# Performance work log

Hardware: AMD Instinct MI355X
Metric: run time of the kernel (lower is better)

Reference implementation:

```python
import jax, jax.numpy as jnp
import numpy as np

B, N, D, NS, ITERS = 32, 2048, 512, 8, 3
EPS = 1e-8
SCALE = D ** -0.5
LN_EPS = 1e-5


def _ln(x, g, b):
    m = x.mean(-1, keepdims=True)
    v = ((x - m) ** 2).mean(-1, keepdims=True)
    return (x - m) * jax.lax.rsqrt(v + LN_EPS) * g + b


def setup_inputs() -> dict:
    key = jax.random.key(0)
    ks = iter(jax.random.split(key, 40))
    w = lambda *s: jax.random.normal(next(ks), s, jnp.float32) * 0.02
    inp = {
        'inputs': jax.random.normal(next(ks), (B, N, D), jnp.float32),
        'slot_noise': jax.random.normal(next(ks), (B, NS, D), jnp.float32),
        'slots_mu': jax.random.normal(next(ks), (1, 1, D), jnp.float32),
        'slots_logsigma': w(1, 1, D),
        'k_w': w(D, D), 'k_b': jnp.zeros((D,), jnp.float32),
        'v_w': w(D, D), 'v_b': jnp.zeros((D,), jnp.float32),
        'gru_w_ih': w(3 * D, D), 'gru_w_hh': w(3 * D, D),
        'gru_b_ih': jnp.zeros((3 * D,), jnp.float32),
        'gru_b_hh': jnp.zeros((3 * D,), jnp.float32),
        'ln_in_g': jnp.ones((D,), jnp.float32), 'ln_in_b': jnp.zeros((D,), jnp.float32),
        'ln_slots_g': jnp.ones((D,), jnp.float32), 'ln_slots_b': jnp.zeros((D,), jnp.float32),
        'ln_pre_g': jnp.ones((D,), jnp.float32), 'ln_pre_b': jnp.zeros((D,), jnp.float32),
        'mlp1_w': w(1024, D), 'mlp1_b': jnp.zeros((1024,), jnp.float32),
        'mlp2_w': w(1024, 1024), 'mlp2_b': jnp.zeros((1024,), jnp.float32),
        'mlp3_w': w(512, 1024), 'mlp3_b': jnp.zeros((512,), jnp.float32),
        'mlp4_w': w(256, 512), 'mlp4_b': jnp.zeros((256,), jnp.float32),
    }
    return inp


def reference(inputs, slot_noise, slots_mu, slots_logsigma, k_w, k_b, v_w, v_b,
              gru_w_ih, gru_w_hh, gru_b_ih, gru_b_hh,
              ln_in_g, ln_in_b, ln_slots_g, ln_slots_b, ln_pre_g, ln_pre_b,
              mlp1_w, mlp1_b, mlp2_w, mlp2_b, mlp3_w, mlp3_b, mlp4_w, mlp4_b):
    b, n, d = inputs.shape
    # stochastic slot init: mu + exp(logsigma) * noise  -> [b, ns, d]
    slots = slots_mu + jnp.exp(slots_logsigma) * slot_noise
    x = _ln(inputs, ln_in_g, ln_in_b)
    k = x @ k_w.T + k_b
    v = x @ v_w.T + v_b
    updates = slots
    for _ in range(ITERS):
        slots_prev = slots
        q = _ln(slots, ln_slots_g, ln_slots_b)
        dots = jnp.einsum('bid,bjd->bij', q, k) * SCALE  # [b, ns, n]
        attn = jax.nn.softmax(dots, axis=1) + EPS        # softmax over slot axis
        attn = attn / attn.sum(-1, keepdims=True)        # renorm over tokens
        updates = jnp.einsum('bjd,bij->bid', v, attn)    # [b, ns, d]
        # GRUCell(updates, slots_prev), then residual add of updates
        u = updates.reshape(-1, d)
        h = slots_prev.reshape(-1, d)
        gi = u @ gru_w_ih.T + gru_b_ih
        gh = h @ gru_w_hh.T + gru_b_hh
        i_r, i_z, i_n = jnp.split(gi, 3, axis=-1)
        h_r, h_z, h_n = jnp.split(gh, 3, axis=-1)
        r = jax.nn.sigmoid(i_r + h_r)
        z = jax.nn.sigmoid(i_z + h_z)
        nn_ = jnp.tanh(i_n + r * h_n)
        h_new = (1.0 - z) * nn_ + z * h
        slots = (u + h_new).reshape(b, -1, d)
    # output MLP with exact GELU (torch default)
    s = _ln(slots, ln_pre_g, ln_pre_b)
    s = jax.nn.gelu(s @ mlp1_w.T + mlp1_b, approximate=False)
    s = jax.nn.gelu(s @ mlp2_w.T + mlp2_b, approximate=False)
    s = jax.nn.gelu(s @ mlp3_w.T + mlp3_b, approximate=False)
    s = s @ mlp4_w.T + mlp4_b
    return (updates, s)
```

## Files before the change

### kernel.cpp

```cpp
#include <hip/hip_runtime.h>
#include <math.h>

#define Bb 32
#define Nn 2048
#define Dd 512
#define NS 8
#define ITERS 3
#define EPSf 1e-8f
#define SCALEf 0.04419417382415922f
#define LN_EPSf 1e-5f

#define QHS 520
#define PTS 72
#define CHUNKS 32

typedef _Float16 half8 __attribute__((ext_vector_type(8)));
typedef _Float16 half4 __attribute__((ext_vector_type(4)));
typedef float f32x4 __attribute__((ext_vector_type(4)));

__device__ __forceinline__ float waveReduceSum(float v) {
    #pragma unroll
    for (int m = 32; m >= 1; m >>= 1) v += __shfl_xor(v, m);
    return v;
}

__device__ __forceinline__ float gelu_exact(float x) {
    return 0.5f * x * (1.0f + erff(x * 0.7071067811865476f));
}

__device__ __forceinline__ void async_copy16(const _Float16* g, _Float16* l) {
    __builtin_amdgcn_global_load_lds(
        (const __attribute__((address_space(1))) unsigned int*)g,
        (__attribute__((address_space(3))) unsigned int*)l, 16, 0, 0);
}

__global__ __launch_bounds__(256) void megapack_kernel(
    const float* __restrict__ k_w, const float* __restrict__ v_w,
    const float* __restrict__ w_ih, const float* __restrict__ w_hh,
    const float* __restrict__ m1, const float* __restrict__ m2,
    const float* __restrict__ m3, const float* __restrict__ m4,
    _Float16* __restrict__ Bkv, _Float16* __restrict__ Bih, _Float16* __restrict__ Bhh,
    _Float16* __restrict__ Bm1, _Float16* __restrict__ Bm2,
    _Float16* __restrict__ Bm3, _Float16* __restrict__ Bm4) {
    int bid = blockIdx.x, tid = threadIdx.x;
    const float* src; _Float16* dst; int kbits, base;
    if (bid < 2048) {
        int i = bid * 256 + tid;
        Bkv[i] = (_Float16)(i < 262144 ? k_w[i] : v_w[i - 262144]);
        return;
    }
    else if (bid < 5120)  { src = w_ih; dst = Bih; kbits = 9;  base = 2048; }
    else if (bid < 8192)  { src = w_hh; dst = Bhh; kbits = 9;  base = 5120; }
    else if (bid < 10240) { src = m1;   dst = Bm1; kbits = 9;  base = 8192; }
    else if (bid < 14336) { src = m2;   dst = Bm2; kbits = 10; base = 10240; }
    else if (bid < 16384) { src = m3;   dst = Bm3; kbits = 10; base = 14336; }
    else                  { src = m4;   dst = Bm4; kbits = 9;  base = 16384; }
    int e = (bid - base) * 256 + tid;
    int K = 1 << kbits;
    int row = e >> kbits, k = e & (K - 1);
    _Float16 h = (_Float16)src[e];
    _Float16* d = dst + ((size_t)row << (kbits + 1));
    d[k] = h;
    d[K + k] = h;
}

__global__ __launch_bounds__(256) void pack_ln_single_kernel(
    const float* __restrict__ x, const float* __restrict__ g, const float* __restrict__ b,
    _Float16* __restrict__ Ap) {
    int wid = blockIdx.x * 4 + (threadIdx.x >> 6);
    int lane = threadIdx.x & 63;
    const float4* row4 = (const float4*)(x + (size_t)wid * Dd);
    float4 va = row4[lane * 2], vb = row4[lane * 2 + 1];
    float v[8] = {va.x, va.y, va.z, va.w, vb.x, vb.y, vb.z, vb.w};
    float s = 0.f, sq = 0.f;
    #pragma unroll
    for (int t = 0; t < 8; ++t) { s += v[t]; sq += v[t] * v[t]; }
    s = waveReduceSum(s);
    sq = waveReduceSum(sq);
    float m = s * (1.0f / Dd);
    float var = sq * (1.0f / Dd) - m * m;
    float rs = rsqrtf(var + LN_EPSf);
    const float4* g4 = (const float4*)g;
    const float4* b4 = (const float4*)b;
    float4 ga = g4[lane * 2], gb = g4[lane * 2 + 1];
    float4 ba = b4[lane * 2], bb = b4[lane * 2 + 1];
    float gg[8] = {ga.x, ga.y, ga.z, ga.w, gb.x, gb.y, gb.z, gb.w};
    float bbv[8] = {ba.x, ba.y, ba.z, ba.w, bb.x, bb.y, bb.z, bb.w};
    half8 o;
    #pragma unroll
    for (int t = 0; t < 8; ++t) o[t] = (_Float16)((v[t] - m) * rs * gg[t] + bbv[t]);
    *(half8*)(Ap + (size_t)wid * Dd + lane * 8) = o;
}

__global__ __launch_bounds__(256) void slots_init_kernel(
    const float* __restrict__ noise, const float* __restrict__ mu,
    const float* __restrict__ ls, float* __restrict__ slots, _Float16* __restrict__ A2) {
    int idx = blockIdx.x * 256 + threadIdx.x;
    if (idx >= Bb * NS * Dd) return;
    int d = idx & (Dd - 1);
    float val = mu[d] + expf(ls[d]) * noise[idx];
    slots[idx] = val;
    int row = idx >> 9;
    _Float16 hi = (_Float16)val;
    A2[(size_t)(256 + row) * 1024 + d] = hi;
    A2[(size_t)(256 + row) * 1024 + 512 + d] = (_Float16)(val - (float)hi);
}

__device__ __forceinline__ void hgemm128_core(
    const _Float16* __restrict__ A, const _Float16* __restrict__ Bw,
    int K2, f32x4 acc[4][4], _Float16* As, _Float16* Bs) {
    const int tid = threadIdx.x;
    const int w = tid >> 6, lane = tid & 63;
    const int r8 = lane >> 3, seg = lane & 7;
    const int lr = lane & 15, quad = lane >> 4;
    const int wm = w >> 1, wn = w & 1;
    for (int k0 = 0; k0 < K2; k0 += 64) {
        __syncthreads();
        #pragma unroll
        for (int g = 0; g < 4; ++g) {
            int grp = w * 4 + g;
            int row = grp * 8 + r8;
            async_copy16(A + (size_t)row * K2 + k0 + seg * 8, As + grp * 512);
            async_copy16(Bw + (size_t)row * K2 + k0 + seg * 8, Bs + grp * 512);
        }
        __syncthreads();
        #pragma unroll
        for (int kk = 0; kk < 2; ++kk) {
            half8 a[4], b[4];
            #pragma unroll
            for (int t = 0; t < 4; ++t) {
                a[t] = *(const half8*)(As + (wm * 64 + t * 16 + lr) * 64 + kk * 32 + quad * 8);
                b[t] = *(const half8*)(Bs + (wn * 64 + t * 16 + lr) * 64 + kk * 32 + quad * 8);
            }
            #pragma unroll
            for (int mt = 0; mt < 4; ++mt)
                #pragma unroll
                for (int nt = 0; nt < 4; ++nt)
                    acc[mt][nt] = __builtin_amdgcn_mfma_f32_16x16x32_f16(
                        a[mt], b[nt], acc[mt][nt], 0, 0, 0);
        }
    }
}

__global__ __launch_bounds__(256) void kv_hgemm_kernel(
    const _Float16* __restrict__ Apack, const _Float16* __restrict__ Bkv,
    const float* __restrict__ k_b, const float* __restrict__ v_b,
    _Float16* __restrict__ khalf, _Float16* __restrict__ vT) {
    __shared__ _Float16 smem[17408];
    _Float16* As = smem;
    _Float16* Bs = smem + 8192;
    const int f = blockIdx.x;
    const int m0 = ((f & 7) + ((f >> 6) << 3)) * 128;
    const int n0 = ((f >> 3) & 7) * 128;
    f32x4 acc[4][4];
    #pragma unroll
    for (int i = 0; i < 4; ++i)
        #pragma unroll
        for (int j = 0; j < 4; ++j) acc[i][j] = (f32x4){0.f, 0.f, 0.f, 0.f};
    hgemm128_core(Apack + (size_t)m0 * 512, Bkv + (size_t)n0 * 512, 512, acc, As, Bs);
    __syncthreads();
    const int tid = threadIdx.x;
    const int w = tid >> 6, lane = tid & 63;
    const int lr = lane & 15, quad = lane >> 4;
    const int wm = w >> 1, wn = w & 1;
    const bool isK = (n0 < 512);
    #pragma unroll
    for (int mt = 0; mt < 4; ++mt)
        #pragma unroll
        for (int nt = 0; nt < 4; ++nt) {
            int ml = wm * 64 + mt * 16 + quad * 4;
            int nl = wn * 64 + nt * 16 + lr;
            float bv = isK ? k_b[n0 + nl] : v_b[n0 - 512 + nl];
            #pragma unroll
            for (int r = 0; r < 4; ++r) {
                _Float16 h = (_Float16)(acc[mt][nt][r] + bv);
                if (isK) smem[(ml + r) * 136 + nl] = h;
                else     smem[nl * 136 + ml + r] = h;
            }
        }
    __syncthreads();
    int r = tid >> 1, half = tid & 1;
    _Float16* dst;
    if (isK) {
        dst = khalf + (size_t)(m0 + r) * 512 + n0 + half * 64;
    } else {
        int b = m0 >> 11, j0 = m0 & 2047, d0 = n0 - 512;
        dst = vT + ((size_t)b * 512 + d0 + r) * 2048 + j0 + half * 64;
    }
    #pragma unroll
    for (int c = 0; c < 8; ++c)
        *(half8*)(dst + c * 8) = *(const half8*)(smem + r * 136 + half * 64 + c * 8);
}

__global__ __launch_bounds__(256) void attn_kernel(
    const float* __restrict__ slots, const float* __restrict__ ln_g, const float* __restrict__ ln_b,
    const _Float16* __restrict__ khalf, const _Float16* __restrict__ vT,
    float* __restrict__ rawp, float* __restrict__ sumsp) {
    const int b = blockIdx.y, chunk = blockIdx.x;
    __shared__ _Float16 qh[16 * QHS];
    __shared__ _Float16 pT[16 * PTS];
    __shared__ float sums_lds[64];
    const int tid = threadIdx.x, w = tid >> 6, lane = tid & 63;
    const int lr = lane & 15, quad = lane >> 4;

    #pragma unroll
    for (int rr = 0; rr < 2; ++rr) {
        int row = w * 2 + rr;
        const float* sr = slots + ((size_t)b * NS + row) * Dd;
        float v[8]; float s = 0.f, sq = 0.f;
        #pragma unroll
        for (int t = 0; t < 8; ++t) {
            v[t] = sr[t * 64 + lane];
            s += v[t]; sq += v[t] * v[t];
        }
        s = waveReduceSum(s);
        sq = waveReduceSum(sq);
        float m = s * (1.0f / Dd);
        float var = sq * (1.0f / Dd) - m * m;
        float rs = rsqrtf(var + LN_EPSf);
        #pragma unroll
        for (int t = 0; t < 8; ++t) {
            int d = t * 64 + lane;
            qh[row * QHS + d] = (_Float16)(((v[t] - m) * rs * ln_g[d] + ln_b[d]) * SCALEf);
            qh[(row + 8) * QHS + d] = (_Float16)0.f;
        }
    }
    __syncthreads();

    const int j0 = chunk * 64 + w * 16;
    f32x4 dots = (f32x4){0.f, 0.f, 0.f, 0.f};
    for (int ks = 0; ks < 16; ++ks) {
        half8 bq = *(const half8*)(qh + lr * QHS + ks * 32 + quad * 8);
        half8 ak = *(const half8*)(khalf + ((size_t)b * Nn + j0 + lr) * 512 + ks * 32 + quad * 8);
        dots = __builtin_amdgcn_mfma_f32_16x16x32_f16(ak, bq, dots, 0, 0, 0);
    }
    float ssum = 0.f;
    {
        f32x4 d = dots;
        f32x4 mx = d;
        #pragma unroll
        for (int msk = 1; msk <= 4; msk <<= 1) {
            #pragma unroll
            for (int r = 0; r < 4; ++r) mx[r] = fmaxf(mx[r], __shfl_xor(mx[r], msk));
        }
        f32x4 p;
        #pragma unroll
        for (int r = 0; r < 4; ++r) p[r] = __expf(d[r] - mx[r]);
        f32x4 sm = p;
        #pragma unroll
        for (int msk = 1; msk <= 4; msk <<= 1) {
            #pragma unroll
            for (int r = 0; r < 4; ++r) sm[r] += __shfl_xor(sm[r], msk);
        }
        #pragma unroll
        for (int r = 0; r < 4; ++r) {
            _Float16 ph = (_Float16)(p[r] / sm[r] + EPSf);
            pT[lr * PTS + w * 16 + quad * 4 + r] = ph;
            ssum += (float)ph;
        }
    }
    ssum += __shfl_xor(ssum, 16);
    ssum += __shfl_xor(ssum, 32);
    if (lane < 16) sums_lds[w * 16 + lane] = ssum;
    __syncthreads();

    f32x4 acc[8];
    #pragma unroll
    for (int nf = 0; nf < 8; ++nf) acc[nf] = (f32x4){0.f, 0.f, 0.f, 0.f};
    #pragma unroll
    for (int kc = 0; kc < 2; ++kc) {
        half8 ap = *(const half8*)(pT + lr * PTS + kc * 32 + quad * 8);
        #pragma unroll
        for (int nf = 0; nf < 8; ++nf) {
            int dcol = w * 128 + nf * 16 + lr;
            half8 bv = *(const half8*)(vT + ((size_t)b * 512 + dcol) * 2048 + chunk * 64 + kc * 32 + quad * 8);
            acc[nf] = __builtin_amdgcn_mfma_f32_16x16x32_f16(ap, bv, acc[nf], 0, 0, 0);
        }
    }
    if (quad < 2) {
        #pragma unroll
        for (int nf = 0; nf < 8; ++nf) {
            #pragma unroll
            for (int r = 0; r < 4; ++r) {
                int slot = quad * 4 + r;
                rawp[(((size_t)chunk * Bb + b) * NS + slot) * Dd + w * 128 + nf * 16 + lr] = acc[nf][r];
            }
        }
    }
    if (w == 0 && lane < NS) {
        float tot = sums_lds[lane] + sums_lds[16 + lane] + sums_lds[32 + lane] + sums_lds[48 + lane];
        sumsp[((size_t)chunk * Bb + b) * NS + lane] = tot;
    }
}

__global__ __launch_bounds__(256) void finalize_kernel(
    const float* __restrict__ rawp, const float* __restrict__ sumsp,
    float* __restrict__ u, float* __restrict__ out0, _Float16* __restrict__ A2) {
    int idx = blockIdx.x * 256 + threadIdx.x;
    int row = idx >> 9, k = idx & 511;
    float rs = 0.f, ss = 0.f;
    #pragma unroll
    for (int c = 0; c < CHUNKS; ++c) {
        rs += rawp[(size_t)c * 131072 + idx];
        ss += sumsp[c * 256 + row];
    }
    float val = rs / ss;
    u[idx] = val;
    out0[idx] = val;
    _Float16 hi = (_Float16)val;
    A2[(size_t)row * 1024 + k] = hi;
    A2[(size_t)row * 1024 + 512 + k] = (_Float16)(val - (float)hi);
}

__device__ __forceinline__ void hgemm64_core(
    const _Float16* __restrict__ A, const _Float16* __restrict__ Bw,
    int K2, f32x4 acc[2][2], _Float16* As, _Float16* Bs) {
    const int tid = threadIdx.x;
    const int w = tid >> 6, lane = tid & 63;
    const int r8 = lane >> 3, seg = lane & 7;
    const int lr = lane & 15, quad = lane >> 4;
    const int wm = w >> 1, wn = w & 1;
    for (int k0 = 0; k0 < K2; k0 += 64) {
        __syncthreads();
        #pragma unroll
        for (int p = 0; p < 2; ++p) {
            int grp = p * 4 + w;
            int row = grp * 8 + r8;
            async_copy16(A + (size_t)row * K2 + k0 + seg * 8, As + grp * 512);
            async_copy16(Bw + (size_t)row * K2 + k0 + seg * 8, Bs + grp * 512);
        }
        __syncthreads();
        #pragma unroll
        for (int kk = 0; kk < 2; ++kk) {
            half8 a[2], b[2];
            #pragma unroll
            for (int t = 0; t < 2; ++t) {
                a[t] = *(const half8*)(As + (wm * 32 + t * 16 + lr) * 64 + kk * 32 + quad * 8);
                b[t] = *(const half8*)(Bs + (wn * 32 + t * 16 + lr) * 64 + kk * 32 + quad * 8);
            }
            #pragma unroll
            for (int mt = 0; mt < 2; ++mt)
                #pragma unroll
                for (int nt = 0; nt < 2; ++nt)
                    acc[mt][nt] = __builtin_amdgcn_mfma_f32_16x16x32_f16(
                        a[mt], b[nt], acc[mt][nt], 0, 0, 0);
        }
    }
}

template <int ACT, int PACK>
__global__ __launch_bounds__(256) void hgemm64_kernel(
    const _Float16* __restrict__ A, const _Float16* __restrict__ Bw,
    const float* __restrict__ bias, float* __restrict__ C, _Float16* __restrict__ P,
    int K2, int N, int Kp) {
    __shared__ _Float16 As[4096], Bs[4096];
    const int m0 = blockIdx.y * 64, n0 = blockIdx.x * 64;
    f32x4 acc[2][2];
    #pragma unroll
    for (int i = 0; i < 2; ++i)
        #pragma unroll
        for (int j = 0; j < 2; ++j) acc[i][j] = (f32x4){0.f, 0.f, 0.f, 0.f};
    hgemm64_core(A + (size_t)m0 * K2, Bw + (size_t)n0 * K2, K2, acc, As, Bs);
    const int tid = threadIdx.x;
    const int w = tid >> 6, lane = tid & 63;
    const int lr = lane & 15, quad = lane >> 4;
    const int wm = w >> 1, wn = w & 1;
    #pragma unroll
    for (int mt = 0; mt < 2; ++mt)
        #pragma unroll
        for (int nt = 0; nt < 2; ++nt) {
            int n = n0 + wn * 32 + nt * 16 + lr;
            float bv = bias[n];
            #pragma unroll
            for (int r = 0; r < 4; ++r) {
                int m = m0 + wm * 32 + mt * 16 + quad * 4 + r;
                float val = acc[mt][nt][r] + bv;
                if (ACT) val = gelu_exact(val);
                if (PACK) {
                    _Float16 hi = (_Float16)val;
                    P[(size_t)m * 2 * Kp + n] = hi;
                    P[(size_t)m * 2 * Kp + Kp + n] = (_Float16)(val - (float)hi);
                } else {
                    C[(size_t)m * N + n] = val;
                }
            }
        }
}

__global__ __launch_bounds__(256) void gru_gemm_kernel(
    const _Float16* __restrict__ A2, const _Float16* __restrict__ Bih,
    const _Float16* __restrict__ Bhh, const float* __restrict__ b_ih,
    const float* __restrict__ b_hh, float* __restrict__ gi, float* __restrict__ gh) {
    __shared__ _Float16 As[4096], Bs[4096];
    const int by = blockIdx.y;
    const int n0 = blockIdx.x * 64;
    const _Float16* Ap; const _Float16* Bw; const float* bias; float* C;
    if (by < 4) { Ap = A2 + (size_t)by * 64 * 1024;        Bw = Bih; bias = b_ih; C = gi + (size_t)by * 64 * 1536; }
    else        { Ap = A2 + (size_t)(256 + (by - 4) * 64) * 1024; Bw = Bhh; bias = b_hh; C = gh + (size_t)(by - 4) * 64 * 1536; }
    f32x4 acc[2][2];
    #pragma unroll
    for (int i = 0; i < 2; ++i)
        #pragma unroll
        for (int j = 0; j < 2; ++j) acc[i][j] = (f32x4){0.f, 0.f, 0.f, 0.f};
    hgemm64_core(Ap, Bw + (size_t)n0 * 1024, 1024, acc, As, Bs);
    const int tid = threadIdx.x;
    const int w = tid >> 6, lane = tid & 63;
    const int lr = lane & 15, quad = lane >> 4;
    const int wm = w >> 1, wn = w & 1;
    #pragma unroll
    for (int mt = 0; mt < 2; ++mt)
        #pragma unroll
        for (int nt = 0; nt < 2; ++nt) {
            int n = n0 + wn * 32 + nt * 16 + lr;
            float bv = bias[n];
            #pragma unroll
            for (int r = 0; r < 4; ++r) {
                int m = wm * 32 + mt * 16 + quad * 4 + r;
                C[(size_t)m * 1536 + n] = acc[mt][nt][r] + bv;
            }
        }
}

__global__ __launch_bounds__(256) void gru_elem_kernel(
    const float* __restrict__ gi, const float* __restrict__ gh,
    const float* __restrict__ u, float* __restrict__ slots, _Float16* __restrict__ A2,
    const float* __restrict__ lnp_g, const float* __restrict__ lnp_b,
    _Float16* __restrict__ P1, int last) {
    int row = blockIdx.x * 4 + (threadIdx.x >> 6);
    int lane = threadIdx.x & 63;
    const float* gir = gi + (size_t)row * 1536;
    const float* ghr = gh + (size_t)row * 1536;
    float val[8];
    #pragma unroll
    for (int t = 0; t < 8; ++t) {
        int d = t * 64 + lane;
        float ir = gir[d], iz = gir[512 + d], in_ = gir[1024 + d];
        float hr = ghr[d], hz = ghr[512 + d], hn = ghr[1024 + d];
        float r = 1.0f / (1.0f + expf(-(ir + hr)));
        float z = 1.0f / (1.0f + expf(-(iz + hz)));
        float n = tanhf(in_ + r * hn);
        float h = slots[(size_t)row * 512 + d];
        float hnew = (1.0f - z) * n + z * h;
        float vv = u[(size_t)row * 512 + d] + hnew;
        val[t] = vv;
        slots[(size_t)row * 512 + d] = vv;
        _Float16 hi = (_Float16)vv;
        A2[(size_t)(256 + row) * 1024 + d] = hi;
        A2[(size_t)(256 + row) * 1024 + 512 + d] = (_Float16)(vv - (float)hi);
    }
    if (last) {
        float s = 0.f, sq = 0.f;
        #pragma unroll
        for (int t = 0; t < 8; ++t) { s += val[t]; sq += val[t] * val[t]; }
        s = waveReduceSum(s);
        sq = waveReduceSum(sq);
        float m = s * (1.0f / Dd);
        float var = sq * (1.0f / Dd) - m * m;
        float rs = rsqrtf(var + LN_EPSf);
        #pragma unroll
        for (int t = 0; t < 8; ++t) {
            int d = t * 64 + lane;
            float a = (val[t] - m) * rs * lnp_g[d] + lnp_b[d];
            _Float16 hi = (_Float16)a;
            P1[(size_t)row * 1024 + d] = hi;
            P1[(size_t)row * 1024 + 512 + d] = (_Float16)(a - (float)hi);
        }
    }
}

extern "C" void kernel_launch(void* const* d_in, const int* in_sizes, int n_in,
                              void* d_out, int out_size, void* d_ws, size_t ws_size,
                              hipStream_t stream) {
    const float* inputs   = (const float*)d_in[0];
    const float* noise    = (const float*)d_in[1];
    const float* mu       = (const float*)d_in[2];
    const float* lsig     = (const float*)d_in[3];
    const float* k_w      = (const float*)d_in[4];
    const float* k_b      = (const float*)d_in[5];
    const float* v_w      = (const float*)d_in[6];
    const float* v_b      = (const float*)d_in[7];
    const float* w_ih     = (const float*)d_in[8];
    const float* w_hh     = (const float*)d_in[9];
    const float* b_ih     = (const float*)d_in[10];
    const float* b_hh     = (const float*)d_in[11];
    const float* ln_in_g  = (const float*)d_in[12];
    const float* ln_in_b  = (const float*)d_in[13];
    const float* ln_s_g   = (const float*)d_in[14];
    const float* ln_s_b   = (const float*)d_in[15];
    const float* ln_p_g   = (const float*)d_in[16];
    const float* ln_p_b   = (const float*)d_in[17];
    const float* mlp1_w   = (const float*)d_in[18];
    const float* mlp1_b   = (const float*)d_in[19];
    const float* mlp2_w   = (const float*)d_in[20];
    const float* mlp2_b   = (const float*)d_in[21];
    const float* mlp3_w   = (const float*)d_in[22];
    const float* mlp3_b   = (const float*)d_in[23];
    const float* mlp4_w   = (const float*)d_in[24];
    const float* mlp4_b   = (const float*)d_in[25];
    float* out0 = (float*)d_out;
    float* out1 = (float*)d_out + Bb * NS * Dd;

    char* wp = (char*)d_ws;
    auto alloc = [&](size_t bytes) -> void* {
        void* p = (void*)wp;
        wp += (bytes + 255) & ~(size_t)255;
        return p;
    };
    const size_t MR = (size_t)Bb * Nn;
    _Float16* Apack = (_Float16*)alloc(MR * 512 * 2);
    _Float16* khalf = (_Float16*)alloc(MR * 512 * 2);
    _Float16* vT    = (_Float16*)alloc((size_t)Bb * 512 * Nn * 2);
    _Float16* Bkv   = (_Float16*)alloc((size_t)1024 * 512 * 2);
    _Float16* Bih   = (_Float16*)alloc((size_t)1536 * 1024 * 2);
    _Float16* Bhh   = (_Float16*)alloc((size_t)1536 * 1024 * 2);
    _Float16* Bm1   = (_Float16*)alloc((size_t)1024 * 1024 * 2);
    _Float16* Bm2   = (_Float16*)alloc((size_t)1024 * 2048 * 2);
    _Float16* Bm3   = (_Float16*)alloc((size_t)512 * 2048 * 2);
    _Float16* Bm4   = (_Float16*)alloc((size_t)256 * 1024 * 2);
    float* slots    = (float*)alloc((size_t)Bb * NS * Dd * 4);
    float* rawp     = (float*)alloc((size_t)CHUNKS * Bb * NS * Dd * 4);
    float* sumsp    = (float*)alloc((size_t)CHUNKS * Bb * NS * 4);
    float* ubuf     = (float*)alloc((size_t)Bb * NS * Dd * 4);
    float* gi       = (float*)alloc((size_t)Bb * NS * 1536 * 4);
    float* gh       = (float*)alloc((size_t)Bb * NS * 1536 * 4);
    _Float16* A2    = (_Float16*)alloc((size_t)512 * 1024 * 2);
    _Float16* P1    = (_Float16*)alloc((size_t)256 * 1024 * 2);
    _Float16* P2    = (_Float16*)alloc((size_t)256 * 2048 * 2);
    _Float16* P3    = (_Float16*)alloc((size_t)256 * 2048 * 2);
    _Float16* P4    = (_Float16*)alloc((size_t)256 * 1024 * 2);

    megapack_kernel<<<16896, 256, 0, stream>>>(
        k_w, v_w, w_ih, w_hh, mlp1_w, mlp2_w, mlp3_w, mlp4_w,
        Bkv, Bih, Bhh, Bm1, Bm2, Bm3, Bm4);
    pack_ln_single_kernel<<<MR / 4, 256, 0, stream>>>(inputs, ln_in_g, ln_in_b, Apack);
    slots_init_kernel<<<(Bb * NS * Dd) / 256, 256, 0, stream>>>(noise, mu, lsig, slots, A2);

    kv_hgemm_kernel<<<4096, 256, 0, stream>>>(Apack, Bkv, k_b, v_b, khalf, vT);

    for (int it = 0; it < ITERS; ++it) {
        attn_kernel<<<dim3(CHUNKS, Bb), 256, 0, stream>>>(slots, ln_s_g, ln_s_b, khalf, vT, rawp, sumsp);
        finalize_kernel<<<512, 256, 0, stream>>>(rawp, sumsp, ubuf, out0, A2);
        gru_gemm_kernel<<<dim3(24, 8), 256, 0, stream>>>(A2, Bih, Bhh, b_ih, b_hh, gi, gh);
        gru_elem_kernel<<<64, 256, 0, stream>>>(gi, gh, ubuf, slots, A2,
                                                ln_p_g, ln_p_b, P1, it == ITERS - 1 ? 1 : 0);
    }

    hgemm64_kernel<1, 1><<<dim3(16, 4), 256, 0, stream>>>(P1, Bm1, mlp1_b, nullptr, P2, 1024, 1024, 1024);
    hgemm64_kernel<1, 1><<<dim3(16, 4), 256, 0, stream>>>(P2, Bm2, mlp2_b, nullptr, P3, 2048, 1024, 1024);
    hgemm64_kernel<1, 1><<<dim3(8, 4), 256, 0, stream>>>(P3, Bm3, mlp3_b, nullptr, P4, 2048, 512, 512);
    hgemm64_kernel<0, 0><<<dim3(4, 4), 256, 0, stream>>>(P4, Bm4, mlp4_b, out1, nullptr, 1024, 256, 256);
}
```

Baseline: 681.4 us.

## Enlarge KV GEMM tile to 256x128 and drop LDS staging in small GEMMs

The K/V projection GEMM moves from 128x128 to 256x128 tiles with 8x4 MFMA accumulators per wave, halving the grid. The epilogue is now written out in two 128-row passes through shared memory. The small GRU and MLP GEMMs drop LDS staging and __syncthreads, so each wave loads its MFMA fragments straight from global memory. This cuts barrier and launch overhead on latency-bound small GEMMs but raises register pressure in the KV kernel and loses cross-wave reuse of the global loads.

```diff
diff --git a/kernel.cpp b/kernel.cpp
--- a/kernel.cpp
+++ b/kernel.cpp
@@ -15,7 +15,6 @@
 #define CHUNKS 32
 
 typedef _Float16 half8 __attribute__((ext_vector_type(8)));
-typedef _Float16 half4 __attribute__((ext_vector_type(4)));
 typedef float f32x4 __attribute__((ext_vector_type(4)));
 
 __device__ __forceinline__ float waveReduceSum(float v) {
@@ -106,90 +105,93 @@
     A2[(size_t)(256 + row) * 1024 + 512 + d] = (_Float16)(val - (float)hi);
 }
 
-__device__ __forceinline__ void hgemm128_core(
-    const _Float16* __restrict__ A, const _Float16* __restrict__ Bw,
-    int K2, f32x4 acc[4][4], _Float16* As, _Float16* Bs) {
+__global__ __launch_bounds__(256) void kv_hgemm_kernel(
+    const _Float16* __restrict__ Apack, const _Float16* __restrict__ Bkv,
+    const float* __restrict__ k_b, const float* __restrict__ v_b,
+    _Float16* __restrict__ khalf, _Float16* __restrict__ vT) {
+    __shared__ _Float16 smem[24576];
+    _Float16* As = smem;
+    _Float16* Bs = smem + 16384;
+    const int f = blockIdx.x;
+    const int m0 = ((f & 7) + ((f >> 6) << 3)) * 256;
+    const int n0 = ((f >> 3) & 7) * 128;
     const int tid = threadIdx.x;
     const int w = tid >> 6, lane = tid & 63;
     const int r8 = lane >> 3, seg = lane & 7;
     const int lr = lane & 15, quad = lane >> 4;
     const int wm = w >> 1, wn = w & 1;
-    for (int k0 = 0; k0 < K2; k0 += 64) {
+
+    f32x4 acc[8][4];
+    #pragma unroll
+    for (int i = 0; i < 8; ++i)
+        #pragma unroll
+        for (int j = 0; j < 4; ++j) acc[i][j] = (f32x4){0.f, 0.f, 0.f, 0.f};
+
+    for (int k0 = 0; k0 < 512; k0 += 64) {
         __syncthreads();
         #pragma unroll
-        for (int g = 0; g < 4; ++g) {
-            int grp = w * 4 + g;
-            int row = grp * 8 + r8;
-            async_copy16(A + (size_t)row * K2 + k0 + seg * 8, As + grp * 512);
-            async_copy16(Bw + (size_t)row * K2 + k0 + seg * 8, Bs + grp * 512);
+        for (int g = 0; g < 12; ++g) {
+            int grp = w * 12 + g;
+            if (grp < 32) {
+                int row = grp * 8 + r8;
+                async_copy16(Apack + (size_t)(m0 + row) * 512 + k0 + seg * 8, As + grp * 512);
+            } else {
+                int brow = (grp - 32) * 8 + r8;
+                async_copy16(Bkv + (size_t)(n0 + brow) * 512 + k0 + seg * 8, Bs + (grp - 32) * 512);
+            }
         }
         __syncthreads();
         #pragma unroll
         for (int kk = 0; kk < 2; ++kk) {
-            half8 a[4], b[4];
-            #pragma unroll
-            for (int t = 0; t < 4; ++t) {
-                a[t] = *(const half8*)(As + (wm * 64 + t * 16 + lr) * 64 + kk * 32 + quad * 8);
-                b[t] = *(const half8*)(Bs + (wn * 64 + t * 16 + lr) * 64 + kk * 32 + quad * 8);
-            }
-            #pragma unroll
-            for (int mt = 0; mt < 4; ++mt)
+            half8 a[8], b[4];
+            #pragma unroll
+            for (int t = 0; t < 8; ++t)
+                a[t] = *(const half8*)(As + (wm * 128 + t * 16 + lr) * 64 + kk * 32 + quad * 8);
+            #pragma unroll
+            for (int u = 0; u < 4; ++u)
+                b[u] = *(const half8*)(Bs + (wn * 64 + u * 16 + lr) * 64 + kk * 32 + quad * 8);
+            #pragma unroll
+            for (int mt = 0; mt < 8; ++mt)
                 #pragma unroll
                 for (int nt = 0; nt < 4; ++nt)
                     acc[mt][nt] = __builtin_amdgcn_mfma_f32_16x16x32_f16(
                         a[mt], b[nt], acc[mt][nt], 0, 0, 0);
         }
     }
-}
-
-__global__ __launch_bounds__(256) void kv_hgemm_kernel(
-    const _Float16* __restrict__ Apack, const _Float16* __restrict__ Bkv,
-    const float* __restrict__ k_b, const float* __restrict__ v_b,
-    _Float16* __restrict__ khalf, _Float16* __restrict__ vT) {
-    __shared__ _Float16 smem[17408];
-    _Float16* As = smem;
-    _Float16* Bs = smem + 8192;
-    const int f = blockIdx.x;
-    const int m0 = ((f & 7) + ((f >> 6) << 3)) * 128;
-    const int n0 = ((f >> 3) & 7) * 128;
-    f32x4 acc[4][4];
-    #pragma unroll
-    for (int i = 0; i < 4; ++i)
-        #pragma unroll
-        for (int j = 0; j < 4; ++j) acc[i][j] = (f32x4){0.f, 0.f, 0.f, 0.f};
-    hgemm128_core(Apack + (size_t)m0 * 512, Bkv + (size_t)n0 * 512, 512, acc, As, Bs);
-    __syncthreads();
-    const int tid = threadIdx.x;
-    const int w = tid >> 6, lane = tid & 63;
-    const int lr = lane & 15, quad = lane >> 4;
-    const int wm = w >> 1, wn = w & 1;
     const bool isK = (n0 < 512);
-    #pragma unroll
-    for (int mt = 0; mt < 4; ++mt)
-        #pragma unroll
-        for (int nt = 0; nt < 4; ++nt) {
-            int ml = wm * 64 + mt * 16 + quad * 4;
-            int nl = wn * 64 + nt * 16 + lr;
-            float bv = isK ? k_b[n0 + nl] : v_b[n0 - 512 + nl];
-            #pragma unroll
-            for (int r = 0; r < 4; ++r) {
-                _Float16 h = (_Float16)(acc[mt][nt][r] + bv);
-                if (isK) smem[(ml + r) * 136 + nl] = h;
-                else     smem[nl * 136 + ml + r] = h;
-            }
-        }
-    __syncthreads();
-    int r = tid >> 1, half = tid & 1;
-    _Float16* dst;
-    if (isK) {
-        dst = khalf + (size_t)(m0 + r) * 512 + n0 + half * 64;
-    } else {
-        int b = m0 >> 11, j0 = m0 & 2047, d0 = n0 - 512;
-        dst = vT + ((size_t)b * 512 + d0 + r) * 2048 + j0 + half * 64;
-    }
-    #pragma unroll
-    for (int c = 0; c < 8; ++c)
-        *(half8*)(dst + c * 8) = *(const half8*)(smem + r * 136 + half * 64 + c * 8);
+    const int bidx = m0 >> 11;
+    #pragma unroll
+    for (int p = 0; p < 2; ++p) {
+        __syncthreads();
+        if (wm == p) {
+            #pragma unroll
+            for (int mt = 0; mt < 8; ++mt)
+                #pragma unroll
+                for (int nt = 0; nt < 4; ++nt) {
+                    int ml = mt * 16 + quad * 4;
+                    int nl = wn * 64 + nt * 16 + lr;
+                    float bv = isK ? k_b[n0 + nl] : v_b[n0 - 512 + nl];
+                    #pragma unroll
+                    for (int r = 0; r < 4; ++r) {
+                        _Float16 h = (_Float16)(acc[mt][nt][r] + bv);
+                        if (isK) smem[(ml + r) * 136 + nl] = h;
+                        else     smem[nl * 136 + ml + r] = h;
+                    }
+                }
+        }
+        __syncthreads();
+        int r = tid >> 1, half = tid & 1;
+        _Float16* dst;
+        if (isK) {
+            dst = khalf + (size_t)(m0 + p * 128 + r) * 512 + n0 + half * 64;
+        } else {
+            int j0 = (m0 & 2047) + p * 128;
+            dst = vT + ((size_t)bidx * 512 + (n0 - 512) + r) * 2048 + j0 + half * 64;
+        }
+        #pragma unroll
+        for (int c = 0; c < 8; ++c)
+            *(half8*)(dst + c * 8) = *(const half8*)(smem + r * 136 + half * 64 + c * 8);
+    }
 }
 
 __global__ __launch_bounds__(256) void attn_kernel(
@@ -312,68 +314,51 @@
     A2[(size_t)row * 1024 + 512 + k] = (_Float16)(val - (float)hi);
 }
 
-__device__ __forceinline__ void hgemm64_core(
+__device__ __forceinline__ void sgemm_tile(
     const _Float16* __restrict__ A, const _Float16* __restrict__ Bw,
-    int K2, f32x4 acc[2][2], _Float16* As, _Float16* Bs) {
-    const int tid = threadIdx.x;
-    const int w = tid >> 6, lane = tid & 63;
-    const int r8 = lane >> 3, seg = lane & 7;
+    int m0w, int n0w, int K2, f32x4 acc[2][2]) {
+    const int lane = threadIdx.x & 63;
     const int lr = lane & 15, quad = lane >> 4;
-    const int wm = w >> 1, wn = w & 1;
-    for (int k0 = 0; k0 < K2; k0 += 64) {
-        __syncthreads();
-        #pragma unroll
-        for (int p = 0; p < 2; ++p) {
-            int grp = p * 4 + w;
-            int row = grp * 8 + r8;
-            async_copy16(A + (size_t)row * K2 + k0 + seg * 8, As + grp * 512);
-            async_copy16(Bw + (size_t)row * K2 + k0 + seg * 8, Bs + grp * 512);
-        }
-        __syncthreads();
-        #pragma unroll
-        for (int kk = 0; kk < 2; ++kk) {
-            half8 a[2], b[2];
-            #pragma unroll
-            for (int t = 0; t < 2; ++t) {
-                a[t] = *(const half8*)(As + (wm * 32 + t * 16 + lr) * 64 + kk * 32 + quad * 8);
-                b[t] = *(const half8*)(Bs + (wn * 32 + t * 16 + lr) * 64 + kk * 32 + quad * 8);
-            }
-            #pragma unroll
-            for (int mt = 0; mt < 2; ++mt)
-                #pragma unroll
-                for (int nt = 0; nt < 2; ++nt)
-                    acc[mt][nt] = __builtin_amdgcn_mfma_f32_16x16x32_f16(
-                        a[mt], b[nt], acc[mt][nt], 0, 0, 0);
-        }
+    const _Float16* Ap = A + (size_t)(m0w + lr) * K2 + quad * 8;
+    const _Float16* Bp = Bw + (size_t)(n0w + lr) * K2 + quad * 8;
+    const int steps = K2 >> 5;
+    #pragma unroll 4
+    for (int ks = 0; ks < steps; ++ks) {
+        half8 a0 = *(const half8*)(Ap + ks * 32);
+        half8 a1 = *(const half8*)(Ap + (size_t)16 * K2 + ks * 32);
+        half8 b0 = *(const half8*)(Bp + ks * 32);
+        half8 b1 = *(const half8*)(Bp + (size_t)16 * K2 + ks * 32);
+        acc[0][0] = __builtin_amdgcn_mfma_f32_16x16x32_f16(a0, b0, acc[0][0], 0, 0, 0);
+        acc[0][1] = __builtin_amdgcn_mfma_f32_16x16x32_f16(a0, b1, acc[0][1], 0, 0, 0);
+        acc[1][0] = __builtin_amdgcn_mfma_f32_16x16x32_f16(a1, b0, acc[1][0], 0, 0, 0);
+        acc[1][1] = __builtin_amdgcn_mfma_f32_16x16x32_f16(a1, b1, acc[1][1], 0, 0, 0);
     }
 }
 
 template <int ACT, int PACK>
-__global__ __launch_bounds__(256) void hgemm64_kernel(
+__global__ __launch_bounds__(256) void sgemm_kernel(
     const _Float16* __restrict__ A, const _Float16* __restrict__ Bw,
     const float* __restrict__ bias, float* __restrict__ C, _Float16* __restrict__ P,
     int K2, int N, int Kp) {
-    __shared__ _Float16 As[4096], Bs[4096];
-    const int m0 = blockIdx.y * 64, n0 = blockIdx.x * 64;
-    f32x4 acc[2][2];
-    #pragma unroll
-    for (int i = 0; i < 2; ++i)
-        #pragma unroll
-        for (int j = 0; j < 2; ++j) acc[i][j] = (f32x4){0.f, 0.f, 0.f, 0.f};
-    hgemm64_core(A + (size_t)m0 * K2, Bw + (size_t)n0 * K2, K2, acc, As, Bs);
     const int tid = threadIdx.x;
     const int w = tid >> 6, lane = tid & 63;
     const int lr = lane & 15, quad = lane >> 4;
     const int wm = w >> 1, wn = w & 1;
+    f32x4 acc[2][2];
+    #pragma unroll
+    for (int i = 0; i < 2; ++i)
+        #pragma unroll
+        for (int j = 0; j < 2; ++j) acc[i][j] = (f32x4){0.f, 0.f, 0.f, 0.f};
+    sgemm_tile(A, Bw, blockIdx.y * 64 + wm * 32, blockIdx.x * 64 + wn * 32, K2, acc);
     #pragma unroll
     for (int mt = 0; mt < 2; ++mt)
         #pragma unroll
         for (int nt = 0; nt < 2; ++nt) {
-            int n = n0 + wn * 32 + nt * 16 + lr;
+            int n = blockIdx.x * 64 + wn * 32 + nt * 16 + lr;
             float bv = bias[n];
             #pragma unroll
             for (int r = 0; r < 4; ++r) {
-                int m = m0 + wm * 32 + mt * 16 + quad * 4 + r;
+                int m = blockIdx.y * 64 + wm * 32 + mt * 16 + quad * 4 + r;
                 float val = acc[mt][nt][r] + bv;
                 if (ACT) val = gelu_exact(val);
                 if (PACK) {
@@ -391,22 +376,21 @@
     const _Float16* __restrict__ A2, const _Float16* __restrict__ Bih,
     const _Float16* __restrict__ Bhh, const float* __restrict__ b_ih,
     const float* __restrict__ b_hh, float* __restrict__ gi, float* __restrict__ gh) {
-    __shared__ _Float16 As[4096], Bs[4096];
     const int by = blockIdx.y;
     const int n0 = blockIdx.x * 64;
-    const _Float16* Ap; const _Float16* Bw; const float* bias; float* C;
-    if (by < 4) { Ap = A2 + (size_t)by * 64 * 1024;        Bw = Bih; bias = b_ih; C = gi + (size_t)by * 64 * 1536; }
-    else        { Ap = A2 + (size_t)(256 + (by - 4) * 64) * 1024; Bw = Bhh; bias = b_hh; C = gh + (size_t)(by - 4) * 64 * 1536; }
-    f32x4 acc[2][2];
-    #pragma unroll
-    for (int i = 0; i < 2; ++i)
-        #pragma unroll
-        for (int j = 0; j < 2; ++j) acc[i][j] = (f32x4){0.f, 0.f, 0.f, 0.f};
-    hgemm64_core(Ap, Bw + (size_t)n0 * 1024, 1024, acc, As, Bs);
+    const _Float16* Ap; const _Float16* Bw; const float* bias; float* C; int mb;
+    if (by < 4) { Ap = A2;                       Bw = Bih; bias = b_ih; C = gi; mb = by * 64; }
+    else        { Ap = A2 + (size_t)256 * 1024;  Bw = Bhh; bias = b_hh; C = gh; mb = (by - 4) * 64; }
     const int tid = threadIdx.x;
     const int w = tid >> 6, lane = tid & 63;
     const int lr = lane & 15, quad = lane >> 4;
     const int wm = w >> 1, wn = w & 1;
+    f32x4 acc[2][2];
+    #pragma unroll
+    for (int i = 0; i < 2; ++i)
+        #pragma unroll
+        for (int j = 0; j < 2; ++j) acc[i][j] = (f32x4){0.f, 0.f, 0.f, 0.f};
+    sgemm_tile(Ap, Bw, mb + wm * 32, n0 + wn * 32, 1024, acc);
     #pragma unroll
     for (int mt = 0; mt < 2; ++mt)
         #pragma unroll
@@ -415,7 +399,7 @@
             float bv = bias[n];
             #pragma unroll
             for (int r = 0; r < 4; ++r) {
-                int m = wm * 32 + mt * 16 + quad * 4 + r;
+                int m = mb + wm * 32 + mt * 16 + quad * 4 + r;
                 C[(size_t)m * 1536 + n] = acc[mt][nt][r] + bv;
             }
         }
@@ -535,7 +519,7 @@
     pack_ln_single_kernel<<<MR / 4, 256, 0, stream>>>(inputs, ln_in_g, ln_in_b, Apack);
     slots_init_kernel<<<(Bb * NS * Dd) / 256, 256, 0, stream>>>(noise, mu, lsig, slots, A2);
 
-    kv_hgemm_kernel<<<4096, 256, 0, stream>>>(Apack, Bkv, k_b, v_b, khalf, vT);
+    kv_hgemm_kernel<<<2048, 256, 0, stream>>>(Apack, Bkv, k_b, v_b, khalf, vT);
 
     for (int it = 0; it < ITERS; ++it) {
         attn_kernel<<<dim3(CHUNKS, Bb), 256, 0, stream>>>(slots, ln_s_g, ln_s_b, khalf, vT, rawp, sumsp);
@@ -545,8 +529,8 @@
                                                 ln_p_g, ln_p_b, P1, it == ITERS - 1 ? 1 : 0);
     }
 
-    hgemm64_kernel<1, 1><<<dim3(16, 4), 256, 0, stream>>>(P1, Bm1, mlp1_b, nullptr, P2, 1024, 1024, 1024);
-    hgemm64_kernel<1, 1><<<dim3(16, 4), 256, 0, stream>>>(P2, Bm2, mlp2_b, nullptr, P3, 2048, 1024, 1024);
-    hgemm64_kernel<1, 1><<<dim3(8, 4), 256, 0, stream>>>(P3, Bm3, mlp3_b, nullptr, P4, 2048, 512, 512);
-    hgemm64_kernel<0, 0><<<dim3(4, 4), 256, 0, stream>>>(P4, Bm4, mlp4_b, out1, nullptr, 1024, 256, 256);
-}
+    sgemm_kernel<1, 1><<<dim3(16, 4), 256, 0, stream>>>(P1, Bm1, mlp1_b, nullptr, P2, 1024, 1024, 1024);
+    sgemm_kernel<1, 1><<<dim3(16, 4), 256, 0, stream>>>(P2, Bm2, mlp2_b, nullptr, P3, 2048, 1024, 1024);
+    sgemm_kernel<1, 1><<<dim3(8, 4), 256, 0, stream>>>(P3, Bm3, mlp3_b, nullptr, P4, 2048, 512, 512);
+    sgemm_kernel<0, 0><<<dim3(4, 4), 256, 0, stream>>>(P4, Bm4, mlp4_b, out1, nullptr, 1024, 256, 256);
+}
```

New measurement: 818.4 us. +20.1%, slower.

## Precompute slot LayerNorm query once per iteration and double attention chunk size

Applied to the files above, without the earlier changes.

The slot LayerNorm and scaled fp16 query are now computed once per row in slots_init and gru_elem and stored in a global qh buffer. Previously each attention block recomputed them, 32 chunks per batch. attn_kernel now only copies the query into LDS. Each attention block also covers 128 tokens instead of 64 (CHUNKS 32->16), which halves the partial-sum traffic that finalize has to reduce but also halves the grid to 512 blocks. The hgemm128 core is inlined into kv_hgemm.

```diff
diff --git a/kernel.cpp b/kernel.cpp
--- a/kernel.cpp
+++ b/kernel.cpp
@@ -11,11 +11,10 @@
 #define LN_EPSf 1e-5f
 
 #define QHS 520
-#define PTS 72
-#define CHUNKS 32
+#define PTS 136
+#define CHUNKS 16
 
 typedef _Float16 half8 __attribute__((ext_vector_type(8)));
-typedef _Float16 half4 __attribute__((ext_vector_type(4)));
 typedef float f32x4 __attribute__((ext_vector_type(4)));
 
 __device__ __forceinline__ float waveReduceSum(float v) {
@@ -94,51 +93,33 @@
 
 __global__ __launch_bounds__(256) void slots_init_kernel(
     const float* __restrict__ noise, const float* __restrict__ mu,
-    const float* __restrict__ ls, float* __restrict__ slots, _Float16* __restrict__ A2) {
-    int idx = blockIdx.x * 256 + threadIdx.x;
-    if (idx >= Bb * NS * Dd) return;
-    int d = idx & (Dd - 1);
-    float val = mu[d] + expf(ls[d]) * noise[idx];
-    slots[idx] = val;
-    int row = idx >> 9;
-    _Float16 hi = (_Float16)val;
-    A2[(size_t)(256 + row) * 1024 + d] = hi;
-    A2[(size_t)(256 + row) * 1024 + 512 + d] = (_Float16)(val - (float)hi);
-}
-
-__device__ __forceinline__ void hgemm128_core(
-    const _Float16* __restrict__ A, const _Float16* __restrict__ Bw,
-    int K2, f32x4 acc[4][4], _Float16* As, _Float16* Bs) {
-    const int tid = threadIdx.x;
-    const int w = tid >> 6, lane = tid & 63;
-    const int r8 = lane >> 3, seg = lane & 7;
-    const int lr = lane & 15, quad = lane >> 4;
-    const int wm = w >> 1, wn = w & 1;
-    for (int k0 = 0; k0 < K2; k0 += 64) {
-        __syncthreads();
-        #pragma unroll
-        for (int g = 0; g < 4; ++g) {
-            int grp = w * 4 + g;
-            int row = grp * 8 + r8;
-            async_copy16(A + (size_t)row * K2 + k0 + seg * 8, As + grp * 512);
-            async_copy16(Bw + (size_t)row * K2 + k0 + seg * 8, Bs + grp * 512);
-        }
-        __syncthreads();
-        #pragma unroll
-        for (int kk = 0; kk < 2; ++kk) {
-            half8 a[4], b[4];
-            #pragma unroll
-            for (int t = 0; t < 4; ++t) {
-                a[t] = *(const half8*)(As + (wm * 64 + t * 16 + lr) * 64 + kk * 32 + quad * 8);
-                b[t] = *(const half8*)(Bs + (wn * 64 + t * 16 + lr) * 64 + kk * 32 + quad * 8);
-            }
-            #pragma unroll
-            for (int mt = 0; mt < 4; ++mt)
-                #pragma unroll
-                for (int nt = 0; nt < 4; ++nt)
-                    acc[mt][nt] = __builtin_amdgcn_mfma_f32_16x16x32_f16(
-                        a[mt], b[nt], acc[mt][nt], 0, 0, 0);
-        }
+    const float* __restrict__ ls, float* __restrict__ slots, _Float16* __restrict__ A2,
+    const float* __restrict__ lns_g, const float* __restrict__ lns_b,
+    _Float16* __restrict__ qh) {
+    int row = blockIdx.x * 4 + (threadIdx.x >> 6);
+    int lane = threadIdx.x & 63;
+    float val[8];
+    float s = 0.f, sq = 0.f;
+    #pragma unroll
+    for (int t = 0; t < 8; ++t) {
+        int d = t * 64 + lane;
+        float v = mu[d] + expf(ls[d]) * noise[(size_t)row * 512 + d];
+        val[t] = v;
+        s += v; sq += v * v;
+        slots[(size_t)row * 512 + d] = v;
+        _Float16 hi = (_Float16)v;
+        A2[(size_t)(256 + row) * 1024 + d] = hi;
+        A2[(size_t)(256 + row) * 1024 + 512 + d] = (_Float16)(v - (float)hi);
+    }
+    s = waveReduceSum(s);
+    sq = waveReduceSum(sq);
+    float m = s * (1.0f / Dd);
+    float var = sq * (1.0f / Dd) - m * m;
+    float rs = rsqrtf(var + LN_EPSf);
+    #pragma unroll
+    for (int t = 0; t < 8; ++t) {
+        int d = t * 64 + lane;
+        qh[(size_t)row * 512 + d] = (_Float16)(((val[t] - m) * rs * lns_g[d] + lns_b[d]) * SCALEf);
     }
 }
 
@@ -152,17 +133,43 @@
     const int f = blockIdx.x;
     const int m0 = ((f & 7) + ((f >> 6) << 3)) * 128;
     const int n0 = ((f >> 3) & 7) * 128;
-    f32x4 acc[4][4];
-    #pragma unroll
-    for (int i = 0; i < 4; ++i)
-        #pragma unroll
-        for (int j = 0; j < 4; ++j) acc[i][j] = (f32x4){0.f, 0.f, 0.f, 0.f};
-    hgemm128_core(Apack + (size_t)m0 * 512, Bkv + (size_t)n0 * 512, 512, acc, As, Bs);
-    __syncthreads();
     const int tid = threadIdx.x;
     const int w = tid >> 6, lane = tid & 63;
+    const int r8 = lane >> 3, seg = lane & 7;
     const int lr = lane & 15, quad = lane >> 4;
     const int wm = w >> 1, wn = w & 1;
+    f32x4 acc[4][4];
+    #pragma unroll
+    for (int i = 0; i < 4; ++i)
+        #pragma unroll
+        for (int j = 0; j < 4; ++j) acc[i][j] = (f32x4){0.f, 0.f, 0.f, 0.f};
+    for (int k0 = 0; k0 < 512; k0 += 64) {
+        __syncthreads();
+        #pragma unroll
+        for (int g = 0; g < 4; ++g) {
+            int grp = w * 4 + g;
+            int row = grp * 8 + r8;
+            async_copy16(Apack + (size_t)(m0 + row) * 512 + k0 + seg * 8, As + grp * 512);
+            async_copy16(Bkv + (size_t)(n0 + row) * 512 + k0 + seg * 8, Bs + grp * 512);
+        }
+        __syncthreads();
+        #pragma unroll
+        for (int kk = 0; kk < 2; ++kk) {
+            half8 a[4], b[4];
+            #pragma unroll
+            for (int t = 0; t < 4; ++t) {
+                a[t] = *(const half8*)(As + (wm * 64 + t * 16 + lr) * 64 + kk * 32 + quad * 8);
+                b[t] = *(const half8*)(Bs + (wn * 64 + t * 16 + lr) * 64 + kk * 32 + quad * 8);
+            }
+            #pragma unroll
+            for (int mt = 0; mt < 4; ++mt)
+                #pragma unroll
+                for (int nt = 0; nt < 4; ++nt)
+                    acc[mt][nt] = __builtin_amdgcn_mfma_f32_16x16x32_f16(
+                        a[mt], b[nt], acc[mt][nt], 0, 0, 0);
+        }
+    }
+    __syncthreads();
     const bool isK = (n0 < 512);
     #pragma unroll
     for (int mt = 0; mt < 4; ++mt)
@@ -193,7 +200,7 @@
 }
 
 __global__ __launch_bounds__(256) void attn_kernel(
-    const float* __restrict__ slots, const float* __restrict__ ln_g, const float* __restrict__ ln_b,
+    const _Float16* __restrict__ qh_g,
     const _Float16* __restrict__ khalf, const _Float16* __restrict__ vT,
     float* __restrict__ rawp, float* __restrict__ sumsp) {
     const int b = blockIdx.y, chunk = blockIdx.x;
@@ -203,40 +210,33 @@
     const int tid = threadIdx.x, w = tid >> 6, lane = tid & 63;
     const int lr = lane & 15, quad = lane >> 4;
 
-    #pragma unroll
-    for (int rr = 0; rr < 2; ++rr) {
-        int row = w * 2 + rr;
-        const float* sr = slots + ((size_t)b * NS + row) * Dd;
-        float v[8]; float s = 0.f, sq = 0.f;
-        #pragma unroll
-        for (int t = 0; t < 8; ++t) {
-            v[t] = sr[t * 64 + lane];
-            s += v[t]; sq += v[t] * v[t];
-        }
-        s = waveReduceSum(s);
-        sq = waveReduceSum(sq);
-        float m = s * (1.0f / Dd);
-        float var = sq * (1.0f / Dd) - m * m;
-        float rs = rsqrtf(var + LN_EPSf);
-        #pragma unroll
-        for (int t = 0; t < 8; ++t) {
-            int d = t * 64 + lane;
-            qh[row * QHS + d] = (_Float16)(((v[t] - m) * rs * ln_g[d] + ln_b[d]) * SCALEf);
-            qh[(row + 8) * QHS + d] = (_Float16)0.f;
-        }
+    {
+        int r = tid >> 5;
+        int c = (tid & 31) * 16;
+        *(half8*)(qh + r * QHS + c) = *(const half8*)(qh_g + ((size_t)b * NS + r) * 512 + c);
+        *(half8*)(qh + r * QHS + c + 8) = *(const half8*)(qh_g + ((size_t)b * NS + r) * 512 + c + 8);
+        half8 z = {};
+        *(half8*)(qh + (8 + r) * QHS + c) = z;
+        *(half8*)(qh + (8 + r) * QHS + c + 8) = z;
     }
     __syncthreads();
 
-    const int j0 = chunk * 64 + w * 16;
-    f32x4 dots = (f32x4){0.f, 0.f, 0.f, 0.f};
+    const int j0 = chunk * 128 + w * 32;
+    f32x4 dots[2];
+    dots[0] = (f32x4){0.f, 0.f, 0.f, 0.f};
+    dots[1] = (f32x4){0.f, 0.f, 0.f, 0.f};
     for (int ks = 0; ks < 16; ++ks) {
         half8 bq = *(const half8*)(qh + lr * QHS + ks * 32 + quad * 8);
-        half8 ak = *(const half8*)(khalf + ((size_t)b * Nn + j0 + lr) * 512 + ks * 32 + quad * 8);
-        dots = __builtin_amdgcn_mfma_f32_16x16x32_f16(ak, bq, dots, 0, 0, 0);
+        #pragma unroll
+        for (int mf = 0; mf < 2; ++mf) {
+            half8 ak = *(const half8*)(khalf + ((size_t)b * Nn + j0 + mf * 16 + lr) * 512 + ks * 32 + quad * 8);
+            dots[mf] = __builtin_amdgcn_mfma_f32_16x16x32_f16(ak, bq, dots[mf], 0, 0, 0);
+        }
     }
     float ssum = 0.f;
-    {
-        f32x4 d = dots;
+    #pragma unroll
+    for (int mf = 0; mf < 2; ++mf) {
+        f32x4 d = dots[mf];
         f32x4 mx = d;
         #pragma unroll
         for (int msk = 1; msk <= 4; msk <<= 1) {
@@ -255,7 +255,7 @@
         #pragma unroll
         for (int r = 0; r < 4; ++r) {
             _Float16 ph = (_Float16)(p[r] / sm[r] + EPSf);
-            pT[lr * PTS + w * 16 + quad * 4 + r] = ph;
+            pT[lr * PTS + w * 32 + mf * 16 + quad * 4 + r] = ph;
             ssum += (float)ph;
         }
     }
@@ -268,12 +268,12 @@
     #pragma unroll
     for (int nf = 0; nf < 8; ++nf) acc[nf] = (f32x4){0.f, 0.f, 0.f, 0.f};
     #pragma unroll
-    for (int kc = 0; kc < 2; ++kc) {
+    for (int kc = 0; kc < 4; ++kc) {
         half8 ap = *(const half8*)(pT + lr * PTS + kc * 32 + quad * 8);
         #pragma unroll
         for (int nf = 0; nf < 8; ++nf) {
             int dcol = w * 128 + nf * 16 + lr;
-            half8 bv = *(const half8*)(vT + ((size_t)b * 512 + dcol) * 2048 + chunk * 64 + kc * 32 + quad * 8);
+            half8 bv = *(const half8*)(vT + ((size_t)b * 512 + dcol) * 2048 + chunk * 128 + kc * 32 + quad * 8);
             acc[nf] = __builtin_amdgcn_mfma_f32_16x16x32_f16(ap, bv, acc[nf], 0, 0, 0);
         }
     }
@@ -424,6 +424,8 @@
 __global__ __launch_bounds__(256) void gru_elem_kernel(
     const float* __restrict__ gi, const float* __restrict__ gh,
     const float* __restrict__ u, float* __restrict__ slots, _Float16* __restrict__ A2,
+    const float* __restrict__ lns_g, const float* __restrict__ lns_b,
+    _Float16* __restrict__ qh,
     const float* __restrict__ lnp_g, const float* __restrict__ lnp_b,
     _Float16* __restrict__ P1, int last) {
     int row = blockIdx.x * 4 + (threadIdx.x >> 6);
@@ -448,15 +450,22 @@
         A2[(size_t)(256 + row) * 1024 + d] = hi;
         A2[(size_t)(256 + row) * 1024 + 512 + d] = (_Float16)(vv - (float)hi);
     }
-    if (last) {
-        float s = 0.f, sq = 0.f;
-        #pragma unroll
-        for (int t = 0; t < 8; ++t) { s += val[t]; sq += val[t] * val[t]; }
-        s = waveReduceSum(s);
-        sq = waveReduceSum(sq);
-        float m = s * (1.0f / Dd);
-        float var = sq * (1.0f / Dd) - m * m;
-        float rs = rsqrtf(var + LN_EPSf);
+    float s = 0.f, sq = 0.f;
+    #pragma unroll
+    for (int t = 0; t < 8; ++t) { s += val[t]; sq += val[t] * val[t]; }
+    s = waveReduceSum(s);
+    sq = waveReduceSum(sq);
+    float m = s * (1.0f / Dd);
+    float var = sq * (1.0f / Dd) - m * m;
+    float rs = rsqrtf(var + LN_EPSf);
+    if (!last) {
+        #pragma unroll
+        for (int t = 0; t < 8; ++t) {
+            int d = t * 64 + lane;
+            qh[(size_t)row * 512 + d] =
+                (_Float16)(((val[t] - m) * rs * lns_g[d] + lns_b[d]) * SCALEf);
+        }
+    } else {
         #pragma unroll
         for (int t = 0; t < 8; ++t) {
             int d = t * 64 + lane;
@@ -518,6 +527,7 @@
     _Float16* Bm3   = (_Float16*)alloc((size_t)512 * 2048 * 2);
     _Float16* Bm4   = (_Float16*)alloc((size_t)256 * 1024 * 2);
     float* slots    = (float*)alloc((size_t)Bb * NS * Dd * 4);
+    _Float16* qh    = (_Float16*)alloc((size_t)Bb * NS * Dd * 2);
     float* rawp     = (float*)alloc((size_t)CHUNKS * Bb * NS * Dd * 4);
     float* sumsp    = (float*)alloc((size_t)CHUNKS * Bb * NS * 4);
     float* ubuf     = (float*)alloc((size_t)Bb * NS * Dd * 4);
@@ -533,15 +543,16 @@
         k_w, v_w, w_ih, w_hh, mlp1_w, mlp2_w, mlp3_w, mlp4_w,
         Bkv, Bih, Bhh, Bm1, Bm2, Bm3, Bm4);
     pack_ln_single_kernel<<<MR / 4, 256, 0, stream>>>(inputs, ln_in_g, ln_in_b, Apack);
-    slots_init_kernel<<<(Bb * NS * Dd) / 256, 256, 0, stream>>>(noise, mu, lsig, slots, A2);
+    slots_init_kernel<<<64, 256, 0, stream>>>(noise, mu, lsig, slots, A2, ln_s_g, ln_s_b, qh);
 
     kv_hgemm_kernel<<<4096, 256, 0, stream>>>(Apack, Bkv, k_b, v_b, khalf, vT);
 
     for (int it = 0; it < ITERS; ++it) {
-        attn_kernel<<<dim3(CHUNKS, Bb), 256, 0, stream>>>(slots, ln_s_g, ln_s_b, khalf, vT, rawp, sumsp);
+        attn_kernel<<<dim3(CHUNKS, Bb), 256, 0, stream>>>(qh, khalf, vT, rawp, sumsp);
         finalize_kernel<<<512, 256, 0, stream>>>(rawp, sumsp, ubuf, out0, A2);
         gru_gemm_kernel<<<dim3(24, 8), 256, 0, stream>>>(A2, Bih, Bhh, b_ih, b_hh, gi, gh);
         gru_elem_kernel<<<64, 256, 0, stream>>>(gi, gh, ubuf, slots, A2,
+                                                ln_s_g, ln_s_b, qh,
                                                 ln_p_g, ln_p_b, P1, it == ITERS - 1 ? 1 : 0);
     }
 
```

After: 652.6 us. 4.2% less time.
